# Kernel optimization log

Measured on AMD Instinct MI355X. Metric: run time of the kernel, lower is better.

## Reference

```python
import jax, jax.numpy as jnp
import numpy as np

N_X, N_U, N_Y = 256, 32, 32
BATCH, T = 16, 8192
LAM_MIN, LAM_MAX = 0.9, 0.995
B_SCALE, D_SCALE = 0.25, 0.25


def setup_inputs() -> dict:
    key = jax.random.key(0)
    k = jax.random.split(key, 6)
    # Orthogonal Q via QR of a random Gaussian matrix (as in the torch module)
    M = jax.random.normal(k[0], (N_X, N_X), dtype=jnp.float32)
    Q, _ = jnp.linalg.qr(M)
    lam = LAM_MIN + (LAM_MAX - LAM_MIN) * jax.random.uniform(k[1], (N_X,), dtype=jnp.float32)
    Bmat = B_SCALE * jax.random.normal(k[2], (N_X, N_U), dtype=jnp.float32)
    # C picks out the first n_y coordinates (C[i, i] = 1)
    C = jnp.eye(N_Y, N_X, dtype=jnp.float32)
    D = D_SCALE * jax.random.normal(k[3], (N_Y, N_U), dtype=jnp.float32)
    x0 = jax.random.normal(k[4], (BATCH, N_X), dtype=jnp.float32)
    u = jax.random.normal(k[5], (BATCH, T, N_U), dtype=jnp.float32)
    return {"x0": x0, "u": u, "Q": Q, "lam": lam, "Bmat": Bmat, "C": C, "D": D}


def _diag_scan(lam, v):
    """Diagonal linear recurrence x_t = lam * x_{t-1} + v_t (x_0 folded into v[:, 0]).

    lam: (N,), v: (B, T, N) -> states x_1..x_T of shape (B, T, N).
    """
    a = jnp.broadcast_to(lam, v.shape)

    def op(l, r):
        a1, b1 = l
        a2, b2 = r
        return a1 * a2, a2 * b1 + b2

    return jax.lax.associative_scan(op, (a, v), axis=1)[1]


def reference(x0, u, Q, lam, Bmat, C, D):
    Bz = Q.T @ Bmat            # (n_x, n_u) modal input matrix
    Cz = C @ Q                 # (n_y, n_x) modal output matrix
    z0 = x0 @ Q                # (B, n_x)   modal initial state
    v = jnp.einsum('btu,nu->btn', u, Bz)   # (B, T, n_x)
    v = v.at[:, 0].add(lam * z0)            # fold lam * z0 into first step
    z_next = _diag_scan(lam, v)             # (B, T, n_x) = z_1..z_T
    # y_t uses z_t for t = 0..T-1 (states[:, :-1] in the original)
    z_prev = jnp.concatenate([z0[:, None, :], z_next[:, :-1]], axis=1)
    y = jnp.einsum('btn,yn->bty', z_prev, Cz) + jnp.einsum('btu,yu->bty', u, D)
    return y
```

## Files before the change

kernel.cpp:

```cpp
#include <hip/hip_runtime.h>

typedef _Float16 half4_t __attribute__((ext_vector_type(4)));
typedef _Float16 half8_t __attribute__((ext_vector_type(8)));
typedef float f32x4 __attribute__((ext_vector_type(4)));

constexpr int NX = 256, NU = 32, NY = 32, BATCH = 16, T = 8192;
constexpr int NC = 64, L = 128;
constexpr int SUBT = 32, NSUB = L / SUBT;
constexpr int KW = NX + NU;
constexpr int ZROW = 264;
constexpr int VROW = 260;

__global__ __launch_bounds__(256) void k_pre(
    const float* __restrict__ x0, const float* __restrict__ Q,
    const float* __restrict__ Bm, const float* __restrict__ C,
    const float* __restrict__ D,
    _Float16* __restrict__ Bzh, _Float16* __restrict__ Wh, float* __restrict__ z0)
{
    int o = blockIdx.x * 64 + (threadIdx.x >> 2);
    int p = threadIdx.x & 3;
    if (o >= 20480) {
        if (p == 0) {
            int g = o - 20480, iy = g >> 5, j = g & 31;
            Wh[iy * KW + NX + j] = (_Float16)D[iy * NU + j];
        }
        return;
    }
    float s = 0.f;
    int k0 = p * 64;
    if (o < 8192) {
        int n = o >> 5, j = o & 31;
        for (int k = k0; k < k0 + 64; ++k) s = fmaf(Q[k * NX + n], Bm[k * NU + j], s);
    } else if (o < 16384) {
        int g = o - 8192; int iy = g >> 8, nn = g & 255;
        for (int k = k0; k < k0 + 64; ++k) s = fmaf(C[iy * NX + k], Q[k * NX + nn], s);
    } else {
        int g = o - 16384; int b = g >> 8, nn = g & 255;
        for (int k = k0; k < k0 + 64; ++k) s = fmaf(x0[b * NX + k], Q[k * NX + nn], s);
    }
    s += __shfl_xor(s, 1);
    s += __shfl_xor(s, 2);
    if (p == 0) {
        if (o < 8192) {
            Bzh[o] = (_Float16)s;
        } else if (o < 16384) {
            int g = o - 8192; int iy = g >> 8, nn = g & 255;
            Wh[iy * KW + nn] = (_Float16)s;
        } else {
            z0[o - 16384] = s;
        }
    }
}

__global__ __launch_bounds__(256) void k_phase1(
    const float* __restrict__ u, const float* __restrict__ lam,
    const _Float16* __restrict__ Bzh, float* __restrict__ S)
{
    __shared__ __align__(16) _Float16 ut[SUBT][32];
    __shared__ _Float16 vt[SUBT][VROW];

    const int b = blockIdx.x >> 6, c = blockIdx.x & 63, n = threadIdx.x;
    const int wave = n >> 6, lane = n & 63, m16 = lane & 15, quad = lane >> 4;
    const int tw = wave & 1, ng = wave >> 1;

    half8_t bfrag[8];
    #pragma unroll
    for (int i = 0; i < 8; ++i)
        bfrag[i] = *(const half8_t*)&Bzh[(ng * 128 + i * 16 + m16) * NU + quad * 8];

    float ln = lam[n];
    float cur = 0.f;
    const float* ug = u + ((size_t)(b * T) + (size_t)c * L) * NU;

    for (int sub = 0; sub < NSUB; ++sub) {
        {
            float4 uu = *(const float4*)(ug + (size_t)sub * SUBT * NU + n * 4);
            half4_t h; h.x = (_Float16)uu.x; h.y = (_Float16)uu.y;
            h.z = (_Float16)uu.z; h.w = (_Float16)uu.w;
            *(half4_t*)&ut[n >> 3][(n & 7) * 4] = h;
        }
        __syncthreads();
        half8_t af = *(const half8_t*)&ut[tw * 16 + m16][quad * 8];
        #pragma unroll
        for (int i = 0; i < 8; ++i) {
            f32x4 z4 = {0.f, 0.f, 0.f, 0.f};
            f32x4 va = __builtin_amdgcn_mfma_f32_16x16x32_f16(af, bfrag[i], z4, 0, 0, 0);
            int nn = ng * 128 + i * 16 + m16;
            #pragma unroll
            for (int r = 0; r < 4; ++r)
                vt[tw * 16 + quad * 4 + r][nn] = (_Float16)va[r];
        }
        __syncthreads();
        #pragma unroll
        for (int tt = 0; tt < SUBT; ++tt)
            cur = fmaf(ln, cur, (float)vt[tt][n]);
        __syncthreads();
    }
    S[(size_t)blockIdx.x * NX + n] = cur;
}

__global__ __launch_bounds__(256) void k_phase2(
    const float* __restrict__ z0, const float* __restrict__ lam,
    const float* __restrict__ S, float* __restrict__ P)
{
    int b = blockIdx.x, n = threadIdx.x;
    float ln = lam[n], lamL = ln;
    #pragma unroll
    for (int i = 0; i < 7; ++i) lamL *= lamL;
    float cur = z0[b * NX + n];
    P[(size_t)(b * NC) * NX + n] = cur;
    for (int c = 1; c < NC; ++c) {
        cur = fmaf(lamL, cur, S[(size_t)(b * NC + c - 1) * NX + n]);
        P[(size_t)(b * NC + c) * NX + n] = cur;
    }
}

__global__ __launch_bounds__(256) void k_phase3(
    const float* __restrict__ u, const float* __restrict__ lam,
    const _Float16* __restrict__ Bzh, const _Float16* __restrict__ Wh,
    const float* __restrict__ P, float* __restrict__ y)
{
    __shared__ __align__(16) _Float16 ut[SUBT][32];
    __shared__ _Float16 vt[SUBT][VROW];
    __shared__ __align__(16) _Float16 zt[SUBT][ZROW];

    const int b = blockIdx.x >> 6, c = blockIdx.x & 63, n = threadIdx.x;
    const int wave = n >> 6, lane = n & 63, m16 = lane & 15, quad = lane >> 4;
    const int tw = wave & 1, ng = wave >> 1;

    half8_t bfrag[8];
    #pragma unroll
    for (int i = 0; i < 8; ++i)
        bfrag[i] = *(const half8_t*)&Bzh[(ng * 128 + i * 16 + m16) * NU + quad * 8];
    half8_t wfrag[9];
    #pragma unroll
    for (int kk = 0; kk < 9; ++kk)
        wfrag[kk] = *(const half8_t*)&Wh[(ng * 16 + m16) * KW + kk * 32 + quad * 8];

    float ln = lam[n];
    float cur = P[(size_t)(b * NC + c) * NX + n];
    const float* ug = u + ((size_t)(b * T) + (size_t)c * L) * NU;
    float* yg = y + ((size_t)(b * T) + (size_t)c * L) * NY;

    for (int sub = 0; sub < NSUB; ++sub) {
        {
            float4 uu = *(const float4*)(ug + (size_t)sub * SUBT * NU + n * 4);
            half4_t h; h.x = (_Float16)uu.x; h.y = (_Float16)uu.y;
            h.z = (_Float16)uu.z; h.w = (_Float16)uu.w;
            *(half4_t*)&ut[n >> 3][(n & 7) * 4] = h;
        }
        __syncthreads();
        half8_t af = *(const half8_t*)&ut[tw * 16 + m16][quad * 8];
        #pragma unroll
        for (int i = 0; i < 8; ++i) {
            f32x4 z4 = {0.f, 0.f, 0.f, 0.f};
            f32x4 va = __builtin_amdgcn_mfma_f32_16x16x32_f16(af, bfrag[i], z4, 0, 0, 0);
            int nn = ng * 128 + i * 16 + m16;
            #pragma unroll
            for (int r = 0; r < 4; ++r)
                vt[tw * 16 + quad * 4 + r][nn] = (_Float16)va[r];
        }
        __syncthreads();
        #pragma unroll
        for (int tt = 0; tt < SUBT; ++tt) {
            zt[tt][n] = (_Float16)cur;
            cur = fmaf(ln, cur, (float)vt[tt][n]);
        }
        __syncthreads();
        f32x4 acc = {0.f, 0.f, 0.f, 0.f};
        #pragma unroll
        for (int kk = 0; kk < 8; ++kk) {
            half8_t az = *(const half8_t*)&zt[tw * 16 + m16][kk * 32 + quad * 8];
            acc = __builtin_amdgcn_mfma_f32_16x16x32_f16(az, wfrag[kk], acc, 0, 0, 0);
        }
        {
            half8_t au = *(const half8_t*)&ut[tw * 16 + m16][quad * 8];
            acc = __builtin_amdgcn_mfma_f32_16x16x32_f16(au, wfrag[8], acc, 0, 0, 0);
        }
        #pragma unroll
        for (int r = 0; r < 4; ++r)
            yg[(size_t)(sub * SUBT + tw * 16 + quad * 4 + r) * NY + ng * 16 + m16] = acc[r];
        __syncthreads();
    }
}

extern "C" void kernel_launch(void* const* d_in, const int* in_sizes, int n_in,
                              void* d_out, int out_size, void* d_ws, size_t ws_size,
                              hipStream_t stream) {
    (void)in_sizes; (void)n_in; (void)out_size; (void)ws_size;
    const float* x0  = (const float*)d_in[0];
    const float* u   = (const float*)d_in[1];
    const float* Q   = (const float*)d_in[2];
    const float* lam = (const float*)d_in[3];
    const float* Bm  = (const float*)d_in[4];
    const float* C   = (const float*)d_in[5];
    const float* D   = (const float*)d_in[6];
    float* y = (float*)d_out;

    char* ws = (char*)d_ws;
    _Float16* Bzh = (_Float16*)(ws);
    _Float16* Wh  = (_Float16*)(ws + 16384);
    float*    z0  = (float*)(ws + 34816);
    float*    S   = (float*)(ws + 51200);
    float*    P   = (float*)(ws + 51200 + 1048576);

    k_pre   <<<336, 256, 0, stream>>>(x0, Q, Bm, C, D, Bzh, Wh, z0);
    k_phase1<<<BATCH * NC, 256, 0, stream>>>(u, lam, Bzh, S);
    k_phase2<<<BATCH, 256, 0, stream>>>(z0, lam, S, P);
    k_phase3<<<BATCH * NC, 256, 0, stream>>>(u, lam, Bzh, Wh, P, y);
}
```

Measured before the change: 120.6 us.

## Replace serial per-step scans with lambda-weighted MFMA reductions and triangular matmul

Phase 1 drops the 32-step serial recurrence per thread. Each chunk's final state is now a weighted sum of the MFMA outputs, using precomputed lambda powers, followed by cross-lane shuffles. Phase 3 computes the intra-subchunk prefix scan with a lower-triangular ones matrix multiplied on MFMA, applied to inverse-power-scaled inputs and rescaled afterward. It also double-buffers and swizzles the u tile to drop one barrier and avoid bank conflicts. The trade-off is numerical risk: the scaled values (lam^-32 factors) are stored in fp16, which can lose precision or overflow for small lambda.

```diff
diff --git a/kernel.cpp b/kernel.cpp
--- a/kernel.cpp
+++ b/kernel.cpp
@@ -8,8 +8,9 @@
 constexpr int NC = 64, L = 128;
 constexpr int SUBT = 32, NSUB = L / SUBT;
 constexpr int KW = NX + NU;
-constexpr int ZROW = 264;
-constexpr int VROW = 260;
+constexpr int VP = 40;
+constexpr int ZP = 264;
+constexpr int POOLSZ = NX * VP;
 
 __global__ __launch_bounds__(256) void k_pre(
     const float* __restrict__ x0, const float* __restrict__ Q,
@@ -56,47 +57,67 @@
     const float* __restrict__ u, const float* __restrict__ lam,
     const _Float16* __restrict__ Bzh, float* __restrict__ S)
 {
-    __shared__ __align__(16) _Float16 ut[SUBT][32];
-    __shared__ _Float16 vt[SUBT][VROW];
-
-    const int b = blockIdx.x >> 6, c = blockIdx.x & 63, n = threadIdx.x;
-    const int wave = n >> 6, lane = n & 63, m16 = lane & 15, quad = lane >> 4;
-    const int tw = wave & 1, ng = wave >> 1;
-
-    half8_t bfrag[8];
-    #pragma unroll
-    for (int i = 0; i < 8; ++i)
-        bfrag[i] = *(const half8_t*)&Bzh[(ng * 128 + i * 16 + m16) * NU + quad * 8];
-
-    float ln = lam[n];
-    float cur = 0.f;
+    __shared__ __align__(16) _Float16 ut[2][SUBT][32];
+
+    const int b = blockIdx.x >> 6, c = blockIdx.x & 63, tid = threadIdx.x;
+    const int w = tid >> 6, lane = tid & 63, m16 = lane & 15, quad = lane >> 4;
+
+    half8_t bfrag[4];
+    #pragma unroll
+    for (int i = 0; i < 4; ++i)
+        bfrag[i] = *(const half8_t*)&Bzh[((4 * w + i) * 16 + m16) * NU + quad * 8];
+
+    float wr[4][4], wt16[4], l32[4], acc[4];
+    #pragma unroll
+    for (int i = 0; i < 4; ++i) {
+        float la = lam[(4 * w + i) * 16 + m16];
+        float p2 = la * la, p4 = p2 * p2, p8 = p4 * p4, p16 = p8 * p8;
+        float inv1 = 1.0f / la;
+        float inv4 = (inv1 * inv1) * (inv1 * inv1);
+        float pq = 1.0f;
+        if (quad & 1) pq *= inv4;
+        if (quad & 2) pq *= inv4 * inv4;
+        float w0 = (p16 * p8 * p4 * p2 * la) * pq;
+        wr[i][0] = w0;
+        wr[i][1] = w0 * inv1;
+        wr[i][2] = wr[i][1] * inv1;
+        wr[i][3] = wr[i][2] * inv1;
+        wt16[i] = 1.0f / p16;
+        l32[i] = p16 * p16;
+        acc[i] = 0.f;
+    }
+
     const float* ug = u + ((size_t)(b * T) + (size_t)c * L) * NU;
 
     for (int sub = 0; sub < NSUB; ++sub) {
         {
-            float4 uu = *(const float4*)(ug + (size_t)sub * SUBT * NU + n * 4);
+            float4 uu = *(const float4*)(ug + (size_t)sub * SUBT * NU + tid * 4);
+            int tr = tid >> 3, cb = ((tid & 7) * 4 + (tr & 3) * 8) & 31;
             half4_t h; h.x = (_Float16)uu.x; h.y = (_Float16)uu.y;
             h.z = (_Float16)uu.z; h.w = (_Float16)uu.w;
-            *(half4_t*)&ut[n >> 3][(n & 7) * 4] = h;
-        }
-        __syncthreads();
-        half8_t af = *(const half8_t*)&ut[tw * 16 + m16][quad * 8];
-        #pragma unroll
-        for (int i = 0; i < 8; ++i) {
+            *(half4_t*)&ut[sub & 1][tr][cb] = h;
+        }
+        __syncthreads();
+        int rot = (m16 & 3) * 8;
+        half8_t af0 = *(const half8_t*)&ut[sub & 1][m16][(quad * 8 + rot) & 31];
+        half8_t af1 = *(const half8_t*)&ut[sub & 1][16 + m16][(quad * 8 + rot) & 31];
+        #pragma unroll
+        for (int i = 0; i < 4; ++i) {
             f32x4 z4 = {0.f, 0.f, 0.f, 0.f};
-            f32x4 va = __builtin_amdgcn_mfma_f32_16x16x32_f16(af, bfrag[i], z4, 0, 0, 0);
-            int nn = ng * 128 + i * 16 + m16;
-            #pragma unroll
-            for (int r = 0; r < 4; ++r)
-                vt[tw * 16 + quad * 4 + r][nn] = (_Float16)va[r];
-        }
-        __syncthreads();
-        #pragma unroll
-        for (int tt = 0; tt < SUBT; ++tt)
-            cur = fmaf(ln, cur, (float)vt[tt][n]);
-        __syncthreads();
-    }
-    S[(size_t)blockIdx.x * NX + n] = cur;
+            f32x4 v0 = __builtin_amdgcn_mfma_f32_16x16x32_f16(af0, bfrag[i], z4, 0, 0, 0);
+            f32x4 v1 = __builtin_amdgcn_mfma_f32_16x16x32_f16(af1, bfrag[i], z4, 0, 0, 0);
+            float s0 = wr[i][0] * v0[0] + wr[i][1] * v0[1] + wr[i][2] * v0[2] + wr[i][3] * v0[3];
+            float s1 = wr[i][0] * v1[0] + wr[i][1] * v1[1] + wr[i][2] * v1[2] + wr[i][3] * v1[3];
+            acc[i] = fmaf(l32[i], acc[i], fmaf(wt16[i], s1, s0));
+        }
+    }
+    #pragma unroll
+    for (int i = 0; i < 4; ++i) {
+        acc[i] += __shfl_xor(acc[i], 16);
+        acc[i] += __shfl_xor(acc[i], 32);
+    }
+    float out = quad == 0 ? acc[0] : quad == 1 ? acc[1] : quad == 2 ? acc[2] : acc[3];
+    S[(size_t)blockIdx.x * NX + (4 * w + quad) * 16 + m16] = out;
 }
 
 __global__ __launch_bounds__(256) void k_phase2(
@@ -120,67 +141,137 @@
     const _Float16* __restrict__ Bzh, const _Float16* __restrict__ Wh,
     const float* __restrict__ P, float* __restrict__ y)
 {
-    __shared__ __align__(16) _Float16 ut[SUBT][32];
-    __shared__ _Float16 vt[SUBT][VROW];
-    __shared__ __align__(16) _Float16 zt[SUBT][ZROW];
-
-    const int b = blockIdx.x >> 6, c = blockIdx.x & 63, n = threadIdx.x;
-    const int wave = n >> 6, lane = n & 63, m16 = lane & 15, quad = lane >> 4;
-    const int tw = wave & 1, ng = wave >> 1;
-
-    half8_t bfrag[8];
-    #pragma unroll
-    for (int i = 0; i < 8; ++i)
-        bfrag[i] = *(const half8_t*)&Bzh[(ng * 128 + i * 16 + m16) * NU + quad * 8];
+    __shared__ __align__(16) _Float16 ut[2][SUBT][32];
+    __shared__ __align__(16) _Float16 pool[POOLSZ];
+
+    const int b = blockIdx.x >> 6, c = blockIdx.x & 63, tid = threadIdx.x;
+    const int w = tid >> 6, lane = tid & 63, m16 = lane & 15, quad = lane >> 4;
+    const int tw = w & 1, yw = w >> 1;
+
+    half8_t bfrag[4];
+    #pragma unroll
+    for (int i = 0; i < 4; ++i)
+        bfrag[i] = *(const half8_t*)&Bzh[((4 * w + i) * 16 + m16) * NU + quad * 8];
     half8_t wfrag[9];
     #pragma unroll
     for (int kk = 0; kk < 9; ++kk)
-        wfrag[kk] = *(const half8_t*)&Wh[(ng * 16 + m16) * KW + kk * 32 + quad * 8];
-
-    float ln = lam[n];
-    float cur = P[(size_t)(b * NC + c) * NX + n];
+        wfrag[kk] = *(const half8_t*)&Wh[(yw * 16 + m16) * KW + kk * 32 + quad * 8];
+    half8_t triA[2];
+    #pragma unroll
+    for (int tt = 0; tt < 2; ++tt) {
+        #pragma unroll
+        for (int j = 0; j < 8; ++j)
+            triA[tt][j] = (_Float16)((quad * 8 + j < tt * 16 + m16) ? 1.f : 0.f);
+    }
+
+    float lamn[4], inv1[4], iq[4], i16p[4], fq[4], f16p[4], l32[4], p[4];
+    #pragma unroll
+    for (int i = 0; i < 4; ++i) {
+        int ni = (4 * w + i) * 16 + m16;
+        float la = lam[ni];
+        lamn[i] = la;
+        float p2 = la * la, p4 = p2 * p2, p8 = p4 * p4, p16 = p8 * p8;
+        float iv = 1.0f / la;
+        inv1[i] = iv;
+        float iv4 = (iv * iv) * (iv * iv);
+        float pqi = 1.0f, pqf = 1.0f;
+        if (quad & 1) { pqi *= iv4; pqf *= p4; }
+        if (quad & 2) { pqi *= iv4 * iv4; pqf *= p8; }
+        iq[i] = iv * pqi;
+        fq[i] = pqf;
+        i16p[i] = 1.0f / p16;
+        f16p[i] = p16;
+        l32[i] = p16 * p16;
+        p[i] = P[(size_t)(b * NC + c) * NX + ni];
+    }
+
     const float* ug = u + ((size_t)(b * T) + (size_t)c * L) * NU;
     float* yg = y + ((size_t)(b * T) + (size_t)c * L) * NY;
 
     for (int sub = 0; sub < NSUB; ++sub) {
         {
-            float4 uu = *(const float4*)(ug + (size_t)sub * SUBT * NU + n * 4);
+            float4 uu = *(const float4*)(ug + (size_t)sub * SUBT * NU + tid * 4);
+            int tr = tid >> 3, cb = ((tid & 7) * 4 + (tr & 3) * 8) & 31;
             half4_t h; h.x = (_Float16)uu.x; h.y = (_Float16)uu.y;
             h.z = (_Float16)uu.z; h.w = (_Float16)uu.w;
-            *(half4_t*)&ut[n >> 3][(n & 7) * 4] = h;
-        }
-        __syncthreads();
-        half8_t af = *(const half8_t*)&ut[tw * 16 + m16][quad * 8];
-        #pragma unroll
-        for (int i = 0; i < 8; ++i) {
+            *(half4_t*)&ut[sub & 1][tr][cb] = h;
+        }
+        __syncthreads();
+
+        int rot = (m16 & 3) * 8;
+        half8_t af0 = *(const half8_t*)&ut[sub & 1][m16][(quad * 8 + rot) & 31];
+        half8_t af1 = *(const half8_t*)&ut[sub & 1][16 + m16][(quad * 8 + rot) & 31];
+        float partial[4];
+        #pragma unroll
+        for (int i = 0; i < 4; ++i) {
+            int ni = (4 * w + i) * 16 + m16;
             f32x4 z4 = {0.f, 0.f, 0.f, 0.f};
-            f32x4 va = __builtin_amdgcn_mfma_f32_16x16x32_f16(af, bfrag[i], z4, 0, 0, 0);
-            int nn = ng * 128 + i * 16 + m16;
+            f32x4 v0 = __builtin_amdgcn_mfma_f32_16x16x32_f16(af0, bfrag[i], z4, 0, 0, 0);
+            f32x4 v1 = __builtin_amdgcn_mfma_f32_16x16x32_f16(af1, bfrag[i], z4, 0, 0, 0);
+            float ps = 0.f;
+            float sc = iq[i];
+            half4_t h0, h1;
             #pragma unroll
-            for (int r = 0; r < 4; ++r)
-                vt[tw * 16 + quad * 4 + r][nn] = (_Float16)va[r];
-        }
-        __syncthreads();
-        #pragma unroll
-        for (int tt = 0; tt < SUBT; ++tt) {
-            zt[tt][n] = (_Float16)cur;
-            cur = fmaf(ln, cur, (float)vt[tt][n]);
-        }
-        __syncthreads();
+            for (int r = 0; r < 4; ++r) {
+                float a0 = v0[r] * sc;
+                float a1 = v1[r] * (sc * i16p[i]);
+                ps += a0 + a1;
+                h0[r] = (_Float16)a0;
+                h1[r] = (_Float16)a1;
+                sc *= inv1[i];
+            }
+            partial[i] = ps;
+            *(half4_t*)&pool[ni * VP + quad * 4] = h0;
+            *(half4_t*)&pool[ni * VP + 16 + quad * 4] = h1;
+        }
+        __syncthreads();
+
+        f32x4 zp0[4], zp1[4];
+        #pragma unroll
+        for (int i = 0; i < 4; ++i) {
+            int ni = (4 * w + i) * 16 + m16;
+            half8_t bV = *(const half8_t*)&pool[ni * VP + quad * 8];
+            f32x4 z4 = {0.f, 0.f, 0.f, 0.f};
+            zp0[i] = __builtin_amdgcn_mfma_f32_16x16x32_f16(triA[0], bV, z4, 0, 0, 0);
+            zp1[i] = __builtin_amdgcn_mfma_f32_16x16x32_f16(triA[1], bV, z4, 0, 0, 0);
+        }
+        __syncthreads();
+
+        #pragma unroll
+        for (int i = 0; i < 4; ++i) {
+            int ni = (4 * w + i) * 16 + m16;
+            float f = fq[i];
+            #pragma unroll
+            for (int r = 0; r < 4; ++r) {
+                float zv0 = f * (p[i] + zp0[i][r]);
+                float zv1 = (f * f16p[i]) * (p[i] + zp1[i][r]);
+                pool[(quad * 4 + r) * ZP + ni] = (_Float16)zv0;
+                pool[(16 + quad * 4 + r) * ZP + ni] = (_Float16)zv1;
+                f *= lamn[i];
+            }
+        }
+        #pragma unroll
+        for (int i = 0; i < 4; ++i) {
+            float ps = partial[i];
+            ps += __shfl_xor(ps, 16);
+            ps += __shfl_xor(ps, 32);
+            p[i] = l32[i] * (p[i] + ps);
+        }
+        __syncthreads();
+
         f32x4 acc = {0.f, 0.f, 0.f, 0.f};
         #pragma unroll
         for (int kk = 0; kk < 8; ++kk) {
-            half8_t az = *(const half8_t*)&zt[tw * 16 + m16][kk * 32 + quad * 8];
+            half8_t az = *(const half8_t*)&pool[(tw * 16 + m16) * ZP + kk * 32 + quad * 8];
             acc = __builtin_amdgcn_mfma_f32_16x16x32_f16(az, wfrag[kk], acc, 0, 0, 0);
         }
         {
-            half8_t au = *(const half8_t*)&ut[tw * 16 + m16][quad * 8];
+            half8_t au = *(const half8_t*)&ut[sub & 1][tw * 16 + m16][(quad * 8 + rot) & 31];
             acc = __builtin_amdgcn_mfma_f32_16x16x32_f16(au, wfrag[8], acc, 0, 0, 0);
         }
         #pragma unroll
         for (int r = 0; r < 4; ++r)
-            yg[(size_t)(sub * SUBT + tw * 16 + quad * 4 + r) * NY + ng * 16 + m16] = acc[r];
-        __syncthreads();
+            yg[(size_t)(sub * SUBT + tw * 16 + quad * 4 + r) * NY + yw * 16 + m16] = acc[r];
     }
 }
 
```

Measured after the change: 119.8 us. About the same (-0.6%).
